# Performance work log

Measured on AMD Instinct MI355X. Metric: run time of the kernel, lower is better.

Reference implementation:

```python
import jax, jax.numpy as jnp
import numpy as np

B, M, D, E, K, T = 8192, 6, 128, 5, 2, 60
SHARED_W, UNSHARED_W, LB_W = 0.3, 0.7, 0.01

def _gelu(x):
    return jax.nn.gelu(x, approximate=False)

def _mlp3(x, w1, b1, w2, b2, w3, b3):
    h = _gelu(x @ w1 + b1)
    h = _gelu(h @ w2 + b2)
    return h @ w3 + b3

def _expert_stack(x, w1, b1, w2, b2, w3, b3):
    # x: [N, D]; weights stacked over experts e -> grouped GEMMs
    h = _gelu(jnp.einsum('nd,edh->enh', x, w1) + b1[:, None, :])
    h = _gelu(jnp.einsum('enh,ehg->eng', h, w2) + b2[:, None, :])
    return jnp.einsum('eng,ego->eno', h, w3) + b3[:, None, :]

def setup_inputs():
    key = jax.random.key(0)
    ks = iter(jax.random.split(key, 64))
    p = lambda shape, s=0.05: s * jax.random.normal(next(ks), shape, dtype=jnp.float32)
    return {
        'mode_features': jax.random.normal(next(ks), (B, M, D), dtype=jnp.float32),
        'rw1': p((D, 256)), 'rb1': p((256,)), 'rw2': p((256, 128)), 'rb2': p((128,)),
        'rw3': p((128, E)), 'rb3': p((E,)),
        'sh_tw1': p((D, 256)), 'sh_tb1': p((256,)), 'sh_tw2': p((256, 256)), 'sh_tb2': p((256,)),
        'sh_tw3': p((256, T * 2)), 'sh_tb3': p((T * 2,)),
        'sh_sw1': p((D, 128)), 'sh_sb1': p((128,)), 'sh_sw2': p((128, 64)), 'sh_sb2': p((64,)),
        'sh_sw3': p((64, 1)), 'sh_sb3': p((1,)),
        'ex_tw1': p((E, D, 256)), 'ex_tb1': p((E, 256)), 'ex_tw2': p((E, 256, 256)), 'ex_tb2': p((E, 256)),
        'ex_tw3': p((E, 256, T * 2)), 'ex_tb3': p((E, T * 2)),
        'ex_sw1': p((E, D, 128)), 'ex_sb1': p((E, 128)), 'ex_sw2': p((E, 128, 64)), 'ex_sb2': p((E, 64)),
        'ex_sw3': p((E, 64, 1)), 'ex_sb3': p((E, 1)),
    }

def reference(mode_features, rw1, rb1, rw2, rb2, rw3, rb3,
              sh_tw1, sh_tb1, sh_tw2, sh_tb2, sh_tw3, sh_tb3,
              sh_sw1, sh_sb1, sh_sw2, sh_sb2, sh_sw3, sh_sb3,
              ex_tw1, ex_tb1, ex_tw2, ex_tb2, ex_tw3, ex_tb3,
              ex_sw1, ex_sb1, ex_sw2, ex_sb2, ex_sw3, ex_sb3):
    b, m, d = mode_features.shape
    x = mode_features.reshape(b * m, d)
    # router (Dropout is identity in eval mode)
    logits = _mlp3(x, rw1, rb1, rw2, rb2, rw3, rb3)                 # [N, E]
    probs = jax.nn.softmax(logits, axis=-1)
    router_logits = logits.reshape(b, m, E)
    topk_logits, topk_idx = jax.lax.top_k(router_logits, K)         # [B, M, K]
    topk_probs = jax.nn.softmax(topk_logits, axis=-1)
    # shared expert on all tokens
    shared_traj = _mlp3(x, sh_tw1, sh_tb1, sh_tw2, sh_tb2, sh_tw3, sh_tb3).reshape(b, m, T, 2)
    shared_score = _mlp3(x, sh_sw1, sh_sb1, sh_sw2, sh_sb2, sh_sw3, sh_sb3).reshape(b, m)
    # all unshared experts computed densely (torch code also computes these for expert_predictions)
    traj_all = _expert_stack(x, ex_tw1, ex_tb1, ex_tw2, ex_tb2, ex_tw3, ex_tb3).reshape(E, b, m, T, 2)
    score_all = _expert_stack(x, ex_sw1, ex_sb1, ex_sw2, ex_sb2, ex_sw3, ex_sb3).reshape(E, b, m)
    # top-k combine: gather selected expert outputs (same math as the torch dispatch + index_add_)
    traj_bme = jnp.transpose(traj_all, (1, 2, 0, 3, 4))             # [B, M, E, T, 2]
    score_bme = jnp.transpose(score_all, (1, 2, 0))                 # [B, M, E]
    idx5 = jnp.broadcast_to(topk_idx[..., None, None], (b, m, K, T, 2))
    sel_traj = jnp.take_along_axis(traj_bme, idx5, axis=2)          # [B, M, K, T, 2]
    sel_score = jnp.take_along_axis(score_bme, topk_idx, axis=2)    # [B, M, K]
    unshared_traj = jnp.einsum('bmktc,bmk->bmtc', sel_traj, topk_probs)
    unshared_score = jnp.sum(sel_score * topk_probs, axis=-1)
    final_traj = SHARED_W * shared_traj + UNSHARED_W * unshared_traj
    final_score = SHARED_W * shared_score + UNSHARED_W * unshared_score
    # load-balance aux loss
    avg_probs = jnp.mean(probs, axis=0)                             # [E]
    entropy = -jnp.sum(avg_probs * jnp.log(avg_probs + 1e-8))
    l2 = jnp.mean((avg_probs - 1.0 / E) ** 2)
    aux_loss = -entropy * LB_W + 0.01 * l2
    return (final_traj, final_score, router_logits, topk_idx, aux_loss, traj_all, score_all)
```

## Files before the change

kernel.cpp:

```cpp
#include <hip/hip_runtime.h>
#include <hip/hip_bf16.h>
#include <cstdint>
#include <cstddef>

static constexpr int N_TOK = 49152;
static constexpr size_t OFF_TRAJ     = 0;
static constexpr size_t OFF_SCORE    = 5898240;
static constexpr size_t OFF_LOGITS   = 5947392;
static constexpr size_t OFF_IDX      = 6193152;
static constexpr size_t OFF_AUX      = 6291456;
static constexpr size_t OFF_TRAJALL  = 6291457;
static constexpr size_t OFF_SCOREALL = 35782657;

typedef short s16x8 __attribute__((ext_vector_type(8)));
typedef float f32x4 __attribute__((ext_vector_type(4)));
typedef f32x4 f32x4u __attribute__((aligned(4)));
typedef unsigned int u32;
typedef unsigned short u16;

static constexpr u32 O_T1 = 0,      O_T2 = 196608, O_T3 = 589824;
static constexpr u32 O_S1 = 774144, O_S2 = 872448;
static constexpr u32 OB_T1 = 0, OB_T2 = 1536, OB_T3 = 3072, OB_S1 = 3792, OB_S2 = 4560;
static constexpr u32 OW_S3 = 4944, OB_S3 = 5328;

__device__ __forceinline__ float gelu_exact(float x) {
    return 0.5f * x * (1.0f + erff(x * 0.70710678118654752440f));
}
__device__ __forceinline__ float gelu_f(float x) {
    const float u = 1.5957691216057308f * (x + 0.044715f * x * x * x);
    return x / (1.0f + __expf(-u));
}
__device__ __forceinline__ float bf2f(u16 u) {
    return __uint_as_float(((u32)u) << 16);
}
__device__ __forceinline__ u16 f2bf(float v) {
    return ((__hip_bfloat16_raw)__float2bfloat16(v)).x;
}
__device__ __forceinline__ void gload16(const u16* g, u16* l) {
    __builtin_amdgcn_global_load_lds(
        (const __attribute__((address_space(1))) u32*)g,
        (__attribute__((address_space(3))) u32*)l, 16, 0, 0);
}
#define MFMA16(a, b, c) __builtin_amdgcn_mfma_f32_16x16x32_bf16(a, b, c, 0, 0, 0)
#define SBAR() __builtin_amdgcn_sched_barrier(0)

__device__ __forceinline__ s16x8 lds_frag(const u16* buf, int RBu16, int r, int c) {
    return *(const s16x8*)&buf[r * RBu16 + ((c ^ (r & 7)) << 3)];
}
__device__ __forceinline__ void lds_store4(u16* buf, int RBu16, int r, int colb,
                                           float v0, float v1, float v2, float v3) {
    const int ch = (colb >> 3) ^ (r & 7);
    ushort4 st = { f2bf(v0), f2bf(v1), f2bf(v2), f2bf(v3) };
    *(ushort4*)&buf[r * RBu16 + ch * 8 + (colb & 7)] = st;
}

template<bool GELU>
__global__ __launch_bounds__(256)
void mlp_gemm(const float* __restrict__ A, const float* __restrict__ W,
              const float* __restrict__ bias, float* __restrict__ C,
              int Kd, int H)
{
    __shared__ float As[32][128];
    __shared__ float Ws[32][132];

    const int tid  = threadIdx.x;
    const int tx   = tid & 15;
    const int ty   = tid >> 4;
    const int row0 = blockIdx.x * 128;
    const int col0 = blockIdx.y * 128;
    const int lm = tid >> 1;
    const int lk = (tid & 1) * 16;

    float acc[8][8] = {};

    for (int k0 = 0; k0 < Kd; k0 += 32) {
        {
            const float* src = A + (size_t)(row0 + lm) * Kd + k0 + lk;
            #pragma unroll
            for (int q = 0; q < 4; ++q) {
                float4 f = *(const float4*)(src + q * 4);
                As[lk + q * 4 + 0][lm] = f.x;
                As[lk + q * 4 + 1][lm] = f.y;
                As[lk + q * 4 + 2][lm] = f.z;
                As[lk + q * 4 + 3][lm] = f.w;
            }
        }
        {
            #pragma unroll
            for (int q = 0; q < 2; ++q) {
                const float* wsrc = W + (size_t)(k0 + ty + q * 16) * H + col0 + tx * 8;
                float4 g0 = *(const float4*)wsrc;
                float4 g1 = *(const float4*)(wsrc + 4);
                *(float4*)&Ws[ty + q * 16][tx * 8]     = g0;
                *(float4*)&Ws[ty + q * 16][tx * 8 + 4] = g1;
            }
        }
        __syncthreads();
        #pragma unroll
        for (int kk = 0; kk < 32; ++kk) {
            float a[8], w[8];
            *(float4*)&a[0] = *(const float4*)&As[kk][ty * 8];
            *(float4*)&a[4] = *(const float4*)&As[kk][ty * 8 + 4];
            *(float4*)&w[0] = *(const float4*)&Ws[kk][tx * 8];
            *(float4*)&w[4] = *(const float4*)&Ws[kk][tx * 8 + 4];
            #pragma unroll
            for (int i = 0; i < 8; ++i)
                #pragma unroll
                for (int j = 0; j < 8; ++j)
                    acc[i][j] = fmaf(a[i], w[j], acc[i][j]);
        }
        __syncthreads();
    }

    #pragma unroll
    for (int i = 0; i < 8; ++i) {
        const int r = row0 + ty * 8 + i;
        #pragma unroll
        for (int j = 0; j < 8; ++j) {
            const int c = col0 + tx * 8 + j;
            float v = acc[i][j] + bias[c];
            if (GELU) v = gelu_exact(v);
            C[(size_t)r * H + c] = v;
        }
    }
}

__global__ __launch_bounds__(256)
void router_l3post(const float* __restrict__ rh2, const float* __restrict__ w3,
                   const float* __restrict__ b3, float* __restrict__ logits,
                   float* __restrict__ oidx, float* __restrict__ tp,
                   int* __restrict__ ti, float* __restrict__ part)
{
    __shared__ float w3s[640];
    __shared__ float red[256];
    const int tid = threadIdx.x;
    for (int i = tid; i < 640; i += 256) w3s[i] = w3[i];
    __syncthreads();

    const int n = blockIdx.x * 256 + tid;
    const float* h = rh2 + (size_t)n * 128;

    float l[5];
    #pragma unroll
    for (int e = 0; e < 5; ++e) l[e] = b3[e];
    for (int k = 0; k < 128; k += 4) {
        float4 hv = *(const float4*)(h + k);
        #pragma unroll
        for (int e = 0; e < 5; ++e) {
            l[e] = fmaf(hv.x, w3s[(k + 0) * 5 + e], l[e]);
            l[e] = fmaf(hv.y, w3s[(k + 1) * 5 + e], l[e]);
            l[e] = fmaf(hv.z, w3s[(k + 2) * 5 + e], l[e]);
            l[e] = fmaf(hv.w, w3s[(k + 3) * 5 + e], l[e]);
        }
    }
    #pragma unroll
    for (int e = 0; e < 5; ++e) logits[(size_t)n * 5 + e] = l[e];

    float m = l[0];
    #pragma unroll
    for (int e = 1; e < 5; ++e) m = fmaxf(m, l[e]);
    float p[5], s = 0.f;
    #pragma unroll
    for (int e = 0; e < 5; ++e) { p[e] = expf(l[e] - m); s += p[e]; }
    const float inv = 1.0f / s;

    #pragma unroll
    for (int e = 0; e < 5; ++e) {
        red[tid] = p[e] * inv;
        __syncthreads();
        for (int off = 128; off > 0; off >>= 1) {
            if (tid < off) red[tid] += red[tid + off];
            __syncthreads();
        }
        if (tid == 0) part[blockIdx.x * 5 + e] = red[0];
        __syncthreads();
    }

    int i0 = 0; float v0 = l[0];
    #pragma unroll
    for (int e = 1; e < 5; ++e) if (l[e] > v0) { v0 = l[e]; i0 = e; }
    int i1 = -1; float v1 = -1e30f;
    #pragma unroll
    for (int e = 0; e < 5; ++e) if (e != i0 && l[e] > v1) { v1 = l[e]; i1 = e; }

    const float t  = expf(v1 - v0);
    const float q0 = 1.0f / (1.0f + t);
    const float q1 = t / (1.0f + t);

    oidx[(size_t)n * 2]     = (float)i0;
    oidx[(size_t)n * 2 + 1] = (float)i1;
    tp[n * 2] = q0; tp[n * 2 + 1] = q1;
    ti[n * 2] = i0; ti[n * 2 + 1] = i1;
}

__global__ __launch_bounds__(256)
void aux_kernel(const float* __restrict__ part, float* __restrict__ aux)
{
    __shared__ float avg[5];
    const int tid = threadIdx.x;
    if (tid < 5) {
        float s = 0.f;
        for (int b = 0; b < 192; ++b) s += part[b * 5 + tid];
        avg[tid] = s / (float)N_TOK;
    }
    __syncthreads();
    if (tid == 0) {
        float ent = 0.f, l2 = 0.f;
        #pragma unroll
        for (int e = 0; e < 5; ++e) {
            ent -= avg[e] * logf(avg[e] + 1e-8f);
            float d = avg[e] - 0.2f;
            l2 += d * d;
        }
        l2 *= (1.0f / 5.0f);
        aux[0] = -ent * 0.01f + 0.01f * l2;
    }
}

__global__ __launch_bounds__(512, 2)
void expert_traj(const u16* __restrict__ xb, const u16* __restrict__ wtb,
                 const float* __restrict__ biasp, float* __restrict__ out,
                 float* __restrict__ shtraj)
{
    __shared__ u16 xs[64 * 128];
    __shared__ u16 h1[64 * 256];
    __shared__ u16 h2[64 * 256];
    float* h1f = (float*)h1;

    const int tid  = threadIdx.x;
    const int lane = tid & 63;
    const int wave = tid >> 6;
    const int row0 = blockIdx.x * 64;
    const int e    = blockIdx.y;
    const int frow = lane & 15;
    const int kgrp = lane >> 4;
    const int c0   = wave * 32;

    #pragma unroll
    for (int i = 0; i < 2; ++i) {
        const int idx = i * 512 + tid;
        const int r = idx >> 4, c = idx & 15;
        gload16(xb + (size_t)(row0 + r) * 128 + ((c ^ (r & 7)) << 3), &xs[idx * 8]);
    }

    const int col3 = wave * 16 + kgrp * 4;
    const int r3   = (wave * 16 + frow) < 120 ? (wave * 16 + frow) : 119;

    s16x8 wf1[4][2];
    {
        const u16* w1p = wtb + O_T1 + e * 32768;
        #pragma unroll
        for (int n = 0; n < 2; ++n) {
            const u16* p = w1p + (size_t)(c0 + n * 16 + frow) * 128 + kgrp * 8;
            #pragma unroll
            for (int ks = 0; ks < 4; ++ks) wf1[ks][n] = *(const s16x8*)(p + ks * 32);
        }
    }
    SBAR();

    __syncthreads();

    f32x4 acc1[4][2] = {};
    #pragma unroll
    for (int ks = 0; ks < 4; ++ks)
        #pragma unroll
        for (int m = 0; m < 4; ++m) {
            const s16x8 a = lds_frag(xs, 128, m * 16 + frow, ks * 4 + kgrp);
            #pragma unroll
            for (int n = 0; n < 2; ++n)
                acc1[m][n] = MFMA16(wf1[ks][n], a, acc1[m][n]);
        }

    const u16* w2p = wtb + O_T2 + e * 65536;
    s16x8 wf2a[4][2];
    f32x4 bb1[2];
    #pragma unroll
    for (int n = 0; n < 2; ++n) {
        const u16* p = w2p + (size_t)(c0 + n * 16 + frow) * 256 + kgrp * 8;
        #pragma unroll
        for (int ks = 0; ks < 4; ++ks) wf2a[ks][n] = *(const s16x8*)(p + ks * 32);
        bb1[n] = *(const f32x4*)&biasp[OB_T1 + e * 256 + c0 + n * 16 + kgrp * 4];
    }
    SBAR();

    {
        #pragma unroll
        for (int n = 0; n < 2; ++n) {
            const int colb = c0 + n * 16 + kgrp * 4;
            #pragma unroll
            for (int m = 0; m < 4; ++m)
                lds_store4(h1, 256, m * 16 + frow, colb,
                           gelu_f(acc1[m][n][0] + bb1[n][0]),
                           gelu_f(acc1[m][n][1] + bb1[n][1]),
                           gelu_f(acc1[m][n][2] + bb1[n][2]),
                           gelu_f(acc1[m][n][3] + bb1[n][3]));
        }
    }
    __syncthreads();

    s16x8 wf2b[4][2];
    #pragma unroll
    for (int n = 0; n < 2; ++n) {
        const u16* p = w2p + (size_t)(c0 + n * 16 + frow) * 256 + 128 + kgrp * 8;
        #pragma unroll
        for (int ks = 0; ks < 4; ++ks) wf2b[ks][n] = *(const s16x8*)(p + ks * 32);
    }
    SBAR();

    f32x4 acc2[4][2] = {};
    #pragma unroll
    for (int ks = 0; ks < 4; ++ks)
        #pragma unroll
        for (int m = 0; m < 4; ++m) {
            const s16x8 a = lds_frag(h1, 256, m * 16 + frow, ks * 4 + kgrp);
            #pragma unroll
            for (int n = 0; n < 2; ++n)
                acc2[m][n] = MFMA16(wf2a[ks][n], a, acc2[m][n]);
        }
    #pragma unroll
    for (int ks = 0; ks < 4; ++ks)
        #pragma unroll
        for (int m = 0; m < 4; ++m) {
            const s16x8 a = lds_frag(h1, 256, m * 16 + frow, (ks + 4) * 4 + kgrp);
            #pragma unroll
            for (int n = 0; n < 2; ++n)
                acc2[m][n] = MFMA16(wf2b[ks][n], a, acc2[m][n]);
        }

    s16x8 wf3[8];
    f32x4 bb2[2];
    {
        const u16* w3p = wtb + O_T3 + e * 30720 + (size_t)r3 * 256 + kgrp * 8;
        #pragma unroll
        for (int ks = 0; ks < 8; ++ks) wf3[ks] = *(const s16x8*)(w3p + ks * 32);
        #pragma unroll
        for (int n = 0; n < 2; ++n)
            bb2[n] = *(const f32x4*)&biasp[OB_T2 + e * 256 + c0 + n * 16 + kgrp * 4];
    }
    SBAR();

    {
        #pragma unroll
        for (int n = 0; n < 2; ++n) {
            const int colb = c0 + n * 16 + kgrp * 4;
            #pragma unroll
            for (int m = 0; m < 4; ++m)
                lds_store4(h2, 256, m * 16 + frow, colb,
                           gelu_f(acc2[m][n][0] + bb2[n][0]),
                           gelu_f(acc2[m][n][1] + bb2[n][1]),
                           gelu_f(acc2[m][n][2] + bb2[n][2]),
                           gelu_f(acc2[m][n][3] + bb2[n][3]));
        }
    }
    __syncthreads();

    f32x4 bb3 = *(const f32x4u*)&biasp[OB_T3 + e * 120 + (col3 < 120 ? col3 : 116)];

    f32x4 acc3[4] = {};
    #pragma unroll
    for (int ks = 0; ks < 8; ++ks)
        #pragma unroll
        for (int m = 0; m < 4; ++m) {
            const s16x8 a = lds_frag(h2, 256, m * 16 + frow, ks * 4 + kgrp);
            acc3[m] = MFMA16(wf3[ks], a, acc3[m]);
        }

    if (col3 < 120) {
        #pragma unroll
        for (int m = 0; m < 4; ++m) {
            f32x4 v;
            #pragma unroll
            for (int j = 0; j < 4; ++j) v[j] = acc3[m][j] + bb3[j];
            *(f32x4*)&h1f[(m * 16 + frow) * 120 + col3] = v;
        }
    }
    __syncthreads();

    {
        float* dst = (e < 5) ? out + OFF_TRAJALL + ((size_t)e * N_TOK + row0) * 120
                             : shtraj + (size_t)row0 * 120;
        const int head = (int)((16 - (((size_t)dst) & 15)) & 15) >> 2;
        const int nvec = (7680 - head) >> 2;
        const int tail = 7680 - head - (nvec << 2);
        if (tid < head) dst[tid] = h1f[tid];
        if (tid >= 8 && tid < 8 + tail)
            dst[7680 - tail + (tid - 8)] = h1f[7680 - tail + (tid - 8)];
        #pragma unroll
        for (int i = 0; i < 4; ++i) {
            const int v = i * 512 + tid;
            if (v < nvec) {
                const int q = head + v * 4;
                f32x4 val;
                val[0] = h1f[q];     val[1] = h1f[q + 1];
                val[2] = h1f[q + 2]; val[3] = h1f[q + 3];
                *(f32x4*)(dst + q) = val;
            }
        }
    }
}

__global__ __launch_bounds__(256, 4)
void expert_score(const u16* __restrict__ xb, const u16* __restrict__ wtb,
                  const float* __restrict__ biasp, float* __restrict__ out,
                  float* __restrict__ shscore)
{
    __shared__ u16 xs[64 * 128];
    __shared__ u16 s1[64 * 128];
    __shared__ u16 s2[64 * 64];

    const int tid  = threadIdx.x;
    const int lane = tid & 63;
    const int wave = tid >> 6;
    const int row0 = blockIdx.x * 64;
    const int e    = blockIdx.y;
    const int frow = lane & 15;
    const int kgrp = lane >> 4;
    const int c0   = wave * 32;

    #pragma unroll
    for (int i = 0; i < 4; ++i) {
        const int idx = i * 256 + tid;
        const int r = idx >> 4, c = idx & 15;
        gload16(xb + (size_t)(row0 + r) * 128 + ((c ^ (r & 7)) << 3), &xs[idx * 8]);
    }

    const int tok3 = wave * 16 + (lane >> 2);
    const int kc   = lane & 3;

    s16x8 wfa[4][2];
    {
        const u16* wp = wtb + O_S1 + e * 16384;
        #pragma unroll
        for (int n = 0; n < 2; ++n) {
            const u16* p = wp + (size_t)(c0 + n * 16 + frow) * 128 + kgrp * 8;
            #pragma unroll
            for (int ks = 0; ks < 4; ++ks) wfa[ks][n] = *(const s16x8*)(p + ks * 32);
        }
    }
    SBAR();

    __syncthreads();

    f32x4 acc1[4][2] = {};
    #pragma unroll
    for (int ks = 0; ks < 4; ++ks)
        #pragma unroll
        for (int m = 0; m < 4; ++m) {
            const s16x8 a = lds_frag(xs, 128, m * 16 + frow, ks * 4 + kgrp);
            #pragma unroll
            for (int n = 0; n < 2; ++n)
                acc1[m][n] = MFMA16(wfa[ks][n], a, acc1[m][n]);
        }
    s16x8 wfb[4];
    f32x4 bbs1[2];
    {
        const u16* p = wtb + O_S2 + e * 8192 + (size_t)(wave * 16 + frow) * 128 + kgrp * 8;
        #pragma unroll
        for (int ks = 0; ks < 4; ++ks) wfb[ks] = *(const s16x8*)(p + ks * 32);
        #pragma unroll
        for (int n = 0; n < 2; ++n)
            bbs1[n] = *(const f32x4*)&biasp[OB_S1 + e * 128 + c0 + n * 16 + kgrp * 4];
    }
    SBAR();
    {
        #pragma unroll
        for (int n = 0; n < 2; ++n) {
            const int colb = c0 + n * 16 + kgrp * 4;
            #pragma unroll
            for (int m = 0; m < 4; ++m)
                lds_store4(s1, 128, m * 16 + frow, colb,
                           gelu_f(acc1[m][n][0] + bbs1[n][0]),
                           gelu_f(acc1[m][n][1] + bbs1[n][1]),
                           gelu_f(acc1[m][n][2] + bbs1[n][2]),
                           gelu_f(acc1[m][n][3] + bbs1[n][3]));
        }
    }
    __syncthreads();

    f32x4 acc2[4] = {};
    #pragma unroll
    for (int ks = 0; ks < 4; ++ks)
        #pragma unroll
        for (int m = 0; m < 4; ++m) {
            const s16x8 a = lds_frag(s1, 128, m * 16 + frow, ks * 4 + kgrp);
            acc2[m] = MFMA16(wfb[ks], a, acc2[m]);
        }
    {
        const int colb = wave * 16 + kgrp * 4;
        const f32x4 bb = *(const f32x4*)&biasp[OB_S2 + e * 64 + colb];
        #pragma unroll
        for (int m = 0; m < 4; ++m)
            lds_store4(s2, 64, m * 16 + frow, colb,
                       gelu_f(acc2[m][0] + bb[0]),
                       gelu_f(acc2[m][1] + bb[1]),
                       gelu_f(acc2[m][2] + bb[2]),
                       gelu_f(acc2[m][3] + bb[3]));
    }
    __syncthreads();

    {
        const float* w3 = biasp + OW_S3 + e * 64 + kc * 16;
        const s16x8 va = lds_frag(s2, 64, tok3, kc * 2);
        const s16x8 vb = lds_frag(s2, 64, tok3, kc * 2 + 1);
        float p = 0.f;
        #pragma unroll
        for (int j = 0; j < 8; ++j) p = fmaf(bf2f((u16)va[j]), w3[j], p);
        #pragma unroll
        for (int j = 0; j < 8; ++j) p = fmaf(bf2f((u16)vb[j]), w3[8 + j], p);
        p += __shfl_xor(p, 1);
        p += __shfl_xor(p, 2);
        if (kc == 0) {
            const float val = p + biasp[OB_S3 + e];
            if (e < 5) out[OFF_SCOREALL + (size_t)e * N_TOK + row0 + tok3] = val;
            else       shscore[row0 + tok3] = val;
        }
    }
}

__global__ __launch_bounds__(256)
void combine_all(const float* __restrict__ trajall, const float* __restrict__ shtraj,
                 const float* __restrict__ scoreall, const float* __restrict__ shscore,
                 const float* __restrict__ tp, const int* __restrict__ ti,
                 float* __restrict__ ftraj, float* __restrict__ fscore)
{
    const int i4 = blockIdx.x * 256 + threadIdx.x;
    const int n  = i4 / 30;
    const int q4 = (i4 - n * 30) * 4;
    const int i0 = ti[n * 2], i1 = ti[n * 2 + 1];
    const float p0 = tp[n * 2], p1 = tp[n * 2 + 1];

    const f32x4 a = *(const f32x4u*)&trajall[((size_t)i0 * N_TOK + n) * 120 + q4];
    const f32x4 b = *(const f32x4u*)&trajall[((size_t)i1 * N_TOK + n) * 120 + q4];
    const f32x4 s = *(const f32x4*)&shtraj[(size_t)n * 120 + q4];
    f32x4 r;
    #pragma unroll
    for (int j = 0; j < 4; ++j)
        r[j] = 0.3f * s[j] + 0.7f * (p0 * a[j] + p1 * b[j]);
    *(f32x4*)&ftraj[(size_t)n * 120 + q4] = r;

    if (q4 == 0) {
        const float sa = scoreall[(size_t)i0 * N_TOK + n];
        const float sb = scoreall[(size_t)i1 * N_TOK + n];
        fscore[n] = 0.3f * shscore[n] + 0.7f * (p0 * sa + p1 * sb);
    }
}

__global__ __launch_bounds__(256)
void convert_x(const float* __restrict__ x, u16* __restrict__ xb)
{
    const size_t i = ((size_t)blockIdx.x * 256 + threadIdx.x) * 4;
    float4 v = *(const float4*)(x + i);
    ushort4 o;
    o.x = f2bf(v.x); o.y = f2bf(v.y); o.z = f2bf(v.z); o.w = f2bf(v.w);
    *(ushort4*)(xb + i) = o;
}

struct WDesc { const float* src; u32 dstOff; int K, H, nz; };
struct WTable { WDesc d[10]; };

__global__ __launch_bounds__(256)
void convert_w(WTable t, u16* __restrict__ dst)
{
    const WDesc dd = t.d[blockIdx.y];
    const int tilesK = dd.K >> 5;
    const int tilesH = (dd.H + 31) >> 5;
    const int tt = blockIdx.x;
    if (tt >= tilesK * tilesH * dd.nz) return;
    const int e  = tt / (tilesK * tilesH);
    const int r  = tt - e * (tilesK * tilesH);
    const int th = r / tilesK;
    const int tk = r - th * tilesK;

    __shared__ float tile[32][33];
    const int tx = threadIdx.x & 31;
    const int ty = threadIdx.x >> 5;

    #pragma unroll
    for (int i = 0; i < 4; ++i) {
        const int k = tk * 32 + ty + i * 8;
        const int h = th * 32 + tx;
        tile[ty + i * 8][tx] = (h < dd.H)
            ? dd.src[((size_t)e * dd.K + k) * dd.H + h] : 0.0f;
    }
    __syncthreads();
    #pragma unroll
    for (int i = 0; i < 4; ++i) {
        const int h = th * 32 + ty + i * 8;
        const int k = tk * 32 + tx;
        if (h < dd.H)
            dst[dd.dstOff + ((size_t)e * dd.H + h) * dd.K + k] = f2bf(tile[tx][ty + i * 8]);
    }
}

struct CDesc { const float* src; u32 dstOff; u32 n; };
struct CTable { CDesc d[14]; };

__global__ __launch_bounds__(256)
void pack_f32(CTable t, float* __restrict__ dst)
{
    const CDesc dd = t.d[blockIdx.y];
    const u32 i = blockIdx.x * 256 + threadIdx.x;
    if (i < dd.n) dst[dd.dstOff + i] = dd.src[i];
}

extern "C" void kernel_launch(void* const* d_in, const int* in_sizes, int n_in,
                              void* d_out, int out_size, void* d_ws, size_t ws_size,
                              hipStream_t stream)
{
    (void)in_sizes; (void)n_in; (void)out_size; (void)ws_size;

    const float* x   = (const float*)d_in[0];
    const float* rw1 = (const float*)d_in[1];
    const float* rb1 = (const float*)d_in[2];
    const float* rw2 = (const float*)d_in[3];
    const float* rb2 = (const float*)d_in[4];
    const float* rw3 = (const float*)d_in[5];
    const float* rb3 = (const float*)d_in[6];

    float* out = (float*)d_out;
    char* ws = (char*)d_ws;

    u16*   xb      = (u16*)(ws);
    u16*   wtb     = (u16*)(ws + 12582912);
    float* biasp   = (float*)(ws + 14426112);
    float* part    = (float*)(ws + 14447616);
    float* tp      = (float*)(ws + 14451712);
    int*   ti      = (int*)  (ws + 14844928);
    float* shscore = (float*)(ws + 15238144);
    float* shtraj  = (float*)(ws + 15434752);
    float* rh1     = (float*)(ws + 39027712);
    float* rh2     = (float*)(ws + 89359360);

    const dim3 blk(256);

    mlp_gemm<true ><<<dim3(N_TOK / 128, 2), blk, 0, stream>>>(x,   rw1, rb1, rh1, 128, 256);
    mlp_gemm<true ><<<dim3(N_TOK / 128, 1), blk, 0, stream>>>(rh1, rw2, rb2, rh2, 256, 128);
    router_l3post<<<dim3(N_TOK / 256), blk, 0, stream>>>(
        rh2, rw3, rb3, out + OFF_LOGITS, out + OFF_IDX, tp, ti, part);
    aux_kernel<<<dim3(1), blk, 0, stream>>>(part, out + OFF_AUX);

    convert_x<<<dim3(N_TOK * 128 / 1024), blk, 0, stream>>>(x, xb);
    {
        WTable t;
        t.d[0] = { (const float*)d_in[19], O_T1,              128, 256, 5 };
        t.d[1] = { (const float*)d_in[7],  O_T1 + 5 * 32768,  128, 256, 1 };
        t.d[2] = { (const float*)d_in[21], O_T2,              256, 256, 5 };
        t.d[3] = { (const float*)d_in[9],  O_T2 + 5 * 65536,  256, 256, 1 };
        t.d[4] = { (const float*)d_in[23], O_T3,              256, 120, 5 };
        t.d[5] = { (const float*)d_in[11], O_T3 + 5 * 30720,  256, 120, 1 };
        t.d[6] = { (const float*)d_in[25], O_S1,              128, 128, 5 };
        t.d[7] = { (const float*)d_in[13], O_S1 + 5 * 16384,  128, 128, 1 };
        t.d[8] = { (const float*)d_in[27], O_S2,              128,  64, 5 };
        t.d[9] = { (const float*)d_in[15], O_S2 + 5 * 8192,   128,  64, 1 };
        convert_w<<<dim3(320, 10), blk, 0, stream>>>(t, wtb);
    }
    {
        CTable t;
        t.d[0]  = { (const float*)d_in[20], OB_T1,        1280 };
        t.d[1]  = { (const float*)d_in[8],  OB_T1 + 1280,  256 };
        t.d[2]  = { (const float*)d_in[22], OB_T2,        1280 };
        t.d[3]  = { (const float*)d_in[10], OB_T2 + 1280,  256 };
        t.d[4]  = { (const float*)d_in[24], OB_T3,         600 };
        t.d[5]  = { (const float*)d_in[12], OB_T3 + 600,   120 };
        t.d[6]  = { (const float*)d_in[26], OB_S1,         640 };
        t.d[7]  = { (const float*)d_in[14], OB_S1 + 640,   128 };
        t.d[8]  = { (const float*)d_in[28], OB_S2,         320 };
        t.d[9]  = { (const float*)d_in[16], OB_S2 + 320,    64 };
        t.d[10] = { (const float*)d_in[29], OW_S3,         320 };
        t.d[11] = { (const float*)d_in[17], OW_S3 + 320,    64 };
        t.d[12] = { (const float*)d_in[30], OB_S3,           5 };
        t.d[13] = { (const float*)d_in[18], OB_S3 + 5,       1 };
        pack_f32<<<dim3(5, 14), blk, 0, stream>>>(t, biasp);
    }

    expert_traj <<<dim3(N_TOK / 64, 6), dim3(512), 0, stream>>>(xb, wtb, biasp, out, shtraj);
    expert_score<<<dim3(N_TOK / 64, 6), blk, 0, stream>>>(xb, wtb, biasp, out, shscore);

    combine_all<<<dim3(N_TOK * 30 / 256), blk, 0, stream>>>(
        out + OFF_TRAJALL, shtraj, out + OFF_SCOREALL, shscore,
        tp, ti, out + OFF_TRAJ, out + OFF_SCORE);
}
```

Baseline: 423.3 us.

## Fuse expert score MLP into trajectory kernel and simplify GELU evaluation

Merges the separate expert_score kernel into the expert_traj kernel, so each block reuses the x tile already staged in LDS and the h2 buffer as scratch for the score MLP. This drops one launch and a second global load of the input features. The score layers are remapped onto 8 waves: layer 1 uses one 16-column slice per wave, layer 2 runs on 4 waves, and the final dot product reduces across 8 lanes. The GELU approximation is also refactored to use an FMA and a hardware reciprocal instead of a division. In exchange, the fused kernel holds more registers and has extra barriers.

```diff
diff --git a/kernel.cpp b/kernel.cpp
--- a/kernel.cpp
+++ b/kernel.cpp
@@ -27,8 +27,10 @@
     return 0.5f * x * (1.0f + erff(x * 0.70710678118654752440f));
 }
 __device__ __forceinline__ float gelu_f(float x) {
-    const float u = 1.5957691216057308f * (x + 0.044715f * x * x * x);
-    return x / (1.0f + __expf(-u));
+    const float x2 = x * x;
+    const float u  = x * fmaf(0.07135486172f, x2, 1.5957691216057308f);
+    const float t  = __expf(-u);
+    return x * __builtin_amdgcn_rcpf(1.0f + t);
 }
 __device__ __forceinline__ float bf2f(u16 u) {
     return __uint_as_float(((u32)u) << 16);
@@ -218,14 +220,16 @@
 }
 
 __global__ __launch_bounds__(512, 2)
-void expert_traj(const u16* __restrict__ xb, const u16* __restrict__ wtb,
-                 const float* __restrict__ biasp, float* __restrict__ out,
-                 float* __restrict__ shtraj)
+void expert_fused(const u16* __restrict__ xb, const u16* __restrict__ wtb,
+                  const float* __restrict__ biasp, float* __restrict__ out,
+                  float* __restrict__ shtraj, float* __restrict__ shscore)
 {
     __shared__ u16 xs[64 * 128];
     __shared__ u16 h1[64 * 256];
     __shared__ u16 h2[64 * 256];
     float* h1f = (float*)h1;
+    u16* s1p = h2;
+    u16* s2p = h2 + 64 * 128;
 
     const int tid  = threadIdx.x;
     const int lane = tid & 63;
@@ -354,7 +358,14 @@
     }
     __syncthreads();
 
+    s16x8 wfs1[4];
     f32x4 bb3 = *(const f32x4u*)&biasp[OB_T3 + e * 120 + (col3 < 120 ? col3 : 116)];
+    {
+        const u16* p = wtb + O_S1 + e * 16384 + (size_t)(wave * 16 + frow) * 128 + kgrp * 8;
+        #pragma unroll
+        for (int ks = 0; ks < 4; ++ks) wfs1[ks] = *(const s16x8*)(p + ks * 32);
+    }
+    SBAR();
 
     f32x4 acc3[4] = {};
     #pragma unroll
@@ -397,122 +408,72 @@
             }
         }
     }
-}
-
-__global__ __launch_bounds__(256, 4)
-void expert_score(const u16* __restrict__ xb, const u16* __restrict__ wtb,
-                  const float* __restrict__ biasp, float* __restrict__ out,
-                  float* __restrict__ shscore)
-{
-    __shared__ u16 xs[64 * 128];
-    __shared__ u16 s1[64 * 128];
-    __shared__ u16 s2[64 * 64];
-
-    const int tid  = threadIdx.x;
-    const int lane = tid & 63;
-    const int wave = tid >> 6;
-    const int row0 = blockIdx.x * 64;
-    const int e    = blockIdx.y;
-    const int frow = lane & 15;
-    const int kgrp = lane >> 4;
-    const int c0   = wave * 32;
-
-    #pragma unroll
-    for (int i = 0; i < 4; ++i) {
-        const int idx = i * 256 + tid;
-        const int r = idx >> 4, c = idx & 15;
-        gload16(xb + (size_t)(row0 + r) * 128 + ((c ^ (r & 7)) << 3), &xs[idx * 8]);
-    }
-
-    const int tok3 = wave * 16 + (lane >> 2);
-    const int kc   = lane & 3;
-
-    s16x8 wfa[4][2];
-    {
-        const u16* wp = wtb + O_S1 + e * 16384;
-        #pragma unroll
-        for (int n = 0; n < 2; ++n) {
-            const u16* p = wp + (size_t)(c0 + n * 16 + frow) * 128 + kgrp * 8;
-            #pragma unroll
-            for (int ks = 0; ks < 4; ++ks) wfa[ks][n] = *(const s16x8*)(p + ks * 32);
-        }
-    }
-    SBAR();
-
-    __syncthreads();
-
-    f32x4 acc1[4][2] = {};
+
+    f32x4 accs1[4] = {};
     #pragma unroll
     for (int ks = 0; ks < 4; ++ks)
         #pragma unroll
         for (int m = 0; m < 4; ++m) {
             const s16x8 a = lds_frag(xs, 128, m * 16 + frow, ks * 4 + kgrp);
-            #pragma unroll
-            for (int n = 0; n < 2; ++n)
-                acc1[m][n] = MFMA16(wfa[ks][n], a, acc1[m][n]);
-        }
-    s16x8 wfb[4];
-    f32x4 bbs1[2];
-    {
-        const u16* p = wtb + O_S2 + e * 8192 + (size_t)(wave * 16 + frow) * 128 + kgrp * 8;
-        #pragma unroll
-        for (int ks = 0; ks < 4; ++ks) wfb[ks] = *(const s16x8*)(p + ks * 32);
-        #pragma unroll
-        for (int n = 0; n < 2; ++n)
-            bbs1[n] = *(const f32x4*)&biasp[OB_S1 + e * 128 + c0 + n * 16 + kgrp * 4];
+            accs1[m] = MFMA16(wfs1[ks], a, accs1[m]);
+        }
+    s16x8 wfs2[4];
+    f32x4 bbs1;
+    {
+        const u16* p = wtb + O_S2 + e * 8192 + (size_t)((wave & 3) * 16 + frow) * 128 + kgrp * 8;
+        #pragma unroll
+        for (int ks = 0; ks < 4; ++ks) wfs2[ks] = *(const s16x8*)(p + ks * 32);
+        bbs1 = *(const f32x4*)&biasp[OB_S1 + e * 128 + wave * 16 + kgrp * 4];
     }
     SBAR();
     {
-        #pragma unroll
-        for (int n = 0; n < 2; ++n) {
-            const int colb = c0 + n * 16 + kgrp * 4;
-            #pragma unroll
-            for (int m = 0; m < 4; ++m)
-                lds_store4(s1, 128, m * 16 + frow, colb,
-                           gelu_f(acc1[m][n][0] + bbs1[n][0]),
-                           gelu_f(acc1[m][n][1] + bbs1[n][1]),
-                           gelu_f(acc1[m][n][2] + bbs1[n][2]),
-                           gelu_f(acc1[m][n][3] + bbs1[n][3]));
-        }
-    }
-    __syncthreads();
-
-    f32x4 acc2[4] = {};
-    #pragma unroll
-    for (int ks = 0; ks < 4; ++ks)
-        #pragma unroll
-        for (int m = 0; m < 4; ++m) {
-            const s16x8 a = lds_frag(s1, 128, m * 16 + frow, ks * 4 + kgrp);
-            acc2[m] = MFMA16(wfb[ks], a, acc2[m]);
-        }
-    {
+        const int colb = wave * 16 + kgrp * 4;
+        #pragma unroll
+        for (int m = 0; m < 4; ++m)
+            lds_store4(s1p, 128, m * 16 + frow, colb,
+                       gelu_f(accs1[m][0] + bbs1[0]),
+                       gelu_f(accs1[m][1] + bbs1[1]),
+                       gelu_f(accs1[m][2] + bbs1[2]),
+                       gelu_f(accs1[m][3] + bbs1[3]));
+    }
+    __syncthreads();
+
+    if (wave < 4) {
+        f32x4 accs2[4] = {};
+        #pragma unroll
+        for (int ks = 0; ks < 4; ++ks)
+            #pragma unroll
+            for (int m = 0; m < 4; ++m) {
+                const s16x8 a = lds_frag(s1p, 128, m * 16 + frow, ks * 4 + kgrp);
+                accs2[m] = MFMA16(wfs2[ks], a, accs2[m]);
+            }
         const int colb = wave * 16 + kgrp * 4;
         const f32x4 bb = *(const f32x4*)&biasp[OB_S2 + e * 64 + colb];
         #pragma unroll
         for (int m = 0; m < 4; ++m)
-            lds_store4(s2, 64, m * 16 + frow, colb,
-                       gelu_f(acc2[m][0] + bb[0]),
-                       gelu_f(acc2[m][1] + bb[1]),
-                       gelu_f(acc2[m][2] + bb[2]),
-                       gelu_f(acc2[m][3] + bb[3]));
-    }
-    __syncthreads();
-
-    {
-        const float* w3 = biasp + OW_S3 + e * 64 + kc * 16;
-        const s16x8 va = lds_frag(s2, 64, tok3, kc * 2);
-        const s16x8 vb = lds_frag(s2, 64, tok3, kc * 2 + 1);
+            lds_store4(s2p, 64, m * 16 + frow, colb,
+                       gelu_f(accs2[m][0] + bb[0]),
+                       gelu_f(accs2[m][1] + bb[1]),
+                       gelu_f(accs2[m][2] + bb[2]),
+                       gelu_f(accs2[m][3] + bb[3]));
+    }
+    __syncthreads();
+
+    {
+        const int tok = tid >> 3;
+        const int kc  = tid & 7;
+        const float* w3s = biasp + OW_S3 + e * 64 + kc * 8;
+        const s16x8 v = lds_frag(s2p, 64, tok, kc);
         float p = 0.f;
         #pragma unroll
-        for (int j = 0; j < 8; ++j) p = fmaf(bf2f((u16)va[j]), w3[j], p);
-        #pragma unroll
-        for (int j = 0; j < 8; ++j) p = fmaf(bf2f((u16)vb[j]), w3[8 + j], p);
+        for (int j = 0; j < 8; ++j) p = fmaf(bf2f((u16)v[j]), w3s[j], p);
         p += __shfl_xor(p, 1);
         p += __shfl_xor(p, 2);
+        p += __shfl_xor(p, 4);
         if (kc == 0) {
             const float val = p + biasp[OB_S3 + e];
-            if (e < 5) out[OFF_SCOREALL + (size_t)e * N_TOK + row0 + tok3] = val;
-            else       shscore[row0 + tok3] = val;
+            if (e < 5) out[OFF_SCOREALL + (size_t)e * N_TOK + row0 + tok] = val;
+            else       shscore[row0 + tok] = val;
         }
     }
 }
@@ -673,8 +634,8 @@
         pack_f32<<<dim3(5, 14), blk, 0, stream>>>(t, biasp);
     }
 
-    expert_traj <<<dim3(N_TOK / 64, 6), dim3(512), 0, stream>>>(xb, wtb, biasp, out, shtraj);
-    expert_score<<<dim3(N_TOK / 64, 6), blk, 0, stream>>>(xb, wtb, biasp, out, shscore);
+    expert_fused<<<dim3(N_TOK / 64, 6), dim3(512), 0, stream>>>(
+        xb, wtb, biasp, out, shtraj, shscore);
 
     combine_all<<<dim3(N_TOK * 30 / 256), blk, 0, stream>>>(
         out + OFF_TRAJALL, shtraj, out + OFF_SCOREALL, shscore,
```

New measurement: 390.0 us. -7.9%, faster.
